# Kernel optimization log

Hardware: AMD Instinct MI355X
Metric: run time of the kernel (lower is better)

Reference implementation:

```python
import jax, jax.numpy as jnp
import numpy as np

# ---- static configuration (matches init_kwargs) ----
D_MODEL = 512
N_HEAD = 16
HEAD_DIM = D_MODEL // N_HEAD
SCALE = HEAD_DIM ** -0.5
SIZE = (64, 64)
WINDOW = (8, 8)
SHIFT = (4, 4)
WS = WINDOW[0] * WINDOW[1]          # tokens per window = 64
NW = (SIZE[0] // WINDOW[0]) * (SIZE[1] // WINDOW[1])  # windows per sample = 64


def _rel_pos_index(window):
    w0, w1 = window
    coords = np.stack(np.meshgrid(np.arange(w0), np.arange(w1), indexing='ij')).reshape(2, -1)
    rel = (coords[:, :, None] - coords[:, None, :]).transpose(1, 2, 0)  # [ws, ws, 2]
    rel[:, :, 0] += w0 - 1
    rel[:, :, 1] += w1 - 1
    rel[:, :, 0] *= 2 * w1 - 1
    return rel.sum(-1)  # [ws, ws] in [0, (2w0-1)(2w1-1))


def _shift_mask(size, window, shift):
    # Swin-style attention mask for shifted windows: 1.0 where tokens belong
    # to different cyclic-shift regions, else 0.0. Shape [nw, ws, ws].
    H, W = size
    w0, w1 = window
    s0, s1 = shift
    img = np.zeros((H, W))
    cnt = 0
    h_slices = (slice(0, -w0), slice(-w0, -s0), slice(-s0, None)) if s0 > 0 else (slice(None),)
    w_slices = (slice(0, -w1), slice(-w1, -s1), slice(-s1, None)) if s1 > 0 else (slice(None),)
    for hs in h_slices:
        for ws_ in w_slices:
            img[hs, ws_] = cnt
            cnt += 1
    win = img.reshape(H // w0, w0, W // w1, w1).transpose(0, 2, 1, 3).reshape(-1, w0 * w1)
    return (win[:, None, :] != win[:, :, None]).astype(np.float32)


REL_IDX = jnp.asarray(_rel_pos_index(WINDOW))              # [ws, ws] int
MASK = jnp.asarray(-100.0 * _shift_mask(SIZE, WINDOW, SHIFT))  # [nw, ws, ws]


def setup_inputs() -> dict:
    key = jax.random.key(0)
    k1, k2, k3, k4 = jax.random.split(key, 4)
    x = jax.random.normal(k1, (8, SIZE[0], SIZE[1], D_MODEL), dtype=jnp.float32)
    qkv_w = jax.random.normal(k2, (3 * D_MODEL, D_MODEL), dtype=jnp.float32) * (D_MODEL ** -0.5)
    qkv_b = jax.random.normal(k3, (3 * D_MODEL,), dtype=jnp.float32) * 0.02
    bias_table = jax.random.normal(k4, ((2 * WINDOW[0] - 1) * (2 * WINDOW[1] - 1), N_HEAD), dtype=jnp.float32) * 0.02
    return {"x": x, "qkv_w": qkv_w, "qkv_b": qkv_b, "bias_table": bias_table}


def reference(x, qkv_w, qkv_b, bias_table):
    n, H, W, c = x.shape
    w0, w1 = WINDOW
    # --- window partition: [n, H, W, c] -> [n*nw, ws, c] ---
    part = x.reshape(n, H // w0, w0, W // w1, w1, c)
    part = part.transpose(0, 1, 3, 2, 4, 5).reshape(n * NW, WS, c)
    # --- qkv projection ---
    qkv = (part @ qkv_w.T + qkv_b).reshape(n * NW, WS, 3, N_HEAD, HEAD_DIM)
    q, k, v = qkv[:, :, 0] * SCALE, qkv[:, :, 1], qkv[:, :, 2]
    # --- scores + relative bias + shift mask + softmax ---
    attn = jnp.einsum('wihd,wjhd->whij', q, k)  # [n*nw, nh, ws, ws]
    bias = bias_table[REL_IDX].transpose(2, 0, 1)  # [nh, ws, ws]
    attn = attn.reshape(n, NW, N_HEAD, WS, WS) + bias[None, None] + MASK[None, :, None]
    attn = jax.nn.softmax(attn, axis=-1).reshape(n * NW, N_HEAD, WS, WS)
    # --- AV + unpartition ---
    out = jnp.einsum('whij,wjhd->wihd', attn, v).reshape(n * NW, WS, c)
    out = out.reshape(n, H // w0, W // w1, w0, w1, c)
    return out.transpose(0, 1, 3, 2, 4, 5).reshape(n, H, W, c)
```

## Files before the change

kernel.cpp:

```cpp
#include <hip/hip_runtime.h>
#include <stdint.h>

typedef unsigned short u16;
typedef __attribute__((ext_vector_type(4))) float floatx4;
typedef __attribute__((ext_vector_type(8))) short bf16x8;

#define MTOK   32768
#define KDIM   512
#define NQKV   1536
#define NWIN   512
#define N_HEAD 16
#define SECSZ  (512 * 16 * 2048)
#define QK_SCALE 0.17677669529663687f

__device__ __forceinline__ u16 f2bf(float f) {
  union { float f; unsigned u; } v; v.f = f;
  unsigned r = v.u + 0x7fffu + ((v.u >> 16) & 1u);
  return (u16)(r >> 16);
}

__device__ __forceinline__ void load_lds16(const void* g, void* l) {
  __builtin_amdgcn_global_load_lds((const __attribute__((address_space(1))) void*)g,
                                   (__attribute__((address_space(3))) void*)l,
                                   16, 0, 0);
}

__global__ __launch_bounds__(256) void convert_xw(const float* __restrict__ x,
                                                  const float* __restrict__ wsrc,
                                                  const float* __restrict__ btab,
                                                  u16* __restrict__ A,
                                                  u16* __restrict__ Wb,
                                                  float* __restrict__ tbl) {
  int b = blockIdx.x;
  if (b < 768) {
    int e = (b * 256 + threadIdx.x) * 4;
    const float4 v = *(const float4*)(wsrc + e);
    ushort4 o;
    o.x = f2bf(v.x); o.y = f2bf(v.y); o.z = f2bf(v.z); o.w = f2bf(v.w);
    *(ushort4*)(Wb + e) = o;
  } else if (b < 17152) {
    int idx = (b - 768) * 256 + threadIdx.x;
    int e = idx * 4;
    int c = e & 511;
    int tg = e >> 9;
    int w = tg >> 6, t = tg & 63;
    int img = w >> 6, wy = (w >> 3) & 7, wx = w & 7;
    int ty = t >> 3, tx = t & 7;
    int y = wy * 8 + ty, xp = wx * 8 + tx;
    const float4 v = *(const float4*)(x + (((img * 64 + y) * 64 + xp) * 512 + c));
    ushort4 o;
    o.x = f2bf(v.x); o.y = f2bf(v.y); o.z = f2bf(v.z); o.w = f2bf(v.w);
    *(ushort4*)(A + e) = o;
  } else {
    int q = b - 17152;
    int cls = q >> 4, hh = q & 15;
    int ey = cls >> 1, ex = cls & 1;
    float* To = tbl + (q << 12);
#pragma unroll
    for (int e = 0; e < 16; ++e) {
      int idx = e * 256 + threadIdx.x;
      int i = idx >> 6, j = idx & 63;
      int ty = i >> 3, tx = i & 7, sy = j >> 3, sx = j & 7;
      int ry = ey ? (ty < 4 ? 1 : 2) : 0;
      int rx = ex ? (tx < 4 ? 1 : 2) : 0;
      int qy = ey ? (sy < 4 ? 1 : 2) : 0;
      int qx = ex ? (sx < 4 ? 1 : 2) : 0;
      float v = btab[((ty - sy + 7) * 15 + (tx - sx + 7)) * 16 + hh];
      if (ry * 3 + rx != qy * 3 + qx) v -= 100.0f;
      To[idx] = v;
    }
  }
}

__global__ __launch_bounds__(256, 4) void gemm_qkv(const u16* __restrict__ A,
                                                   const u16* __restrict__ Wb,
                                                   const float* __restrict__ bias,
                                                   u16* __restrict__ QKV) {
  __shared__ __attribute__((aligned(16))) char smem[18432];
  u16* Ct = (u16*)smem;

  int b = blockIdx.x;
  int xcd = b & 7, slot = b >> 3;
  int mtile = (slot / 12) * 8 + xcd;
  int ntile = slot % 12;

  int tid = threadIdx.x;
  int wv = tid >> 6, lane = tid & 63;
  int il = lane & 15, ch = lane >> 4;
  int wm = (wv & 1) * 64, wn = (wv >> 1) * 64;

  floatx4 acc[4][4];
  floatx4 zacc = {0.f, 0.f, 0.f, 0.f};
#pragma unroll
  for (int m = 0; m < 4; ++m)
#pragma unroll
    for (int n = 0; n < 4; ++n) acc[m][n] = zacc;

  int s8   = (tid & 7) ^ ((tid >> 3) & 7);
  int row0 = ((tid >> 3) << 1) + (s8 >> 2);
  int ch4  = s8 & 3;
  const u16* Abase = A + (mtile * 128 + row0) * KDIM + ch4 * 8;
  const u16* Bbase = Wb + (ntile * 128 + row0) * KDIM + ch4 * 8;
  char* lAb = smem;
  char* lBb = smem + 8192;
  char* lA0 = lAb + wv * 1024;
  char* lA1 = lAb + 4096 + wv * 1024;
  char* lB0 = lBb + wv * 1024;
  char* lB1 = lBb + 4096 + wv * 1024;

  int aslot = ((il & 1) * 4 + ch) ^ ((il >> 1) & 7);
  int fbase = (il >> 1) * 128 + aslot * 16;
  int awoff = (wv & 1) * 4096;
  int bwoff = (wv >> 1) * 4096;

  for (int kb = 0; kb < KDIM; kb += 32) {
    __syncthreads();
    load_lds16(Abase + kb, lA0);
    load_lds16(Abase + kb + 64 * KDIM, lA1);
    load_lds16(Bbase + kb, lB0);
    load_lds16(Bbase + kb + 64 * KDIM, lB1);
    __syncthreads();

    bf16x8 af[4], bfr[4];
#pragma unroll
    for (int mt = 0; mt < 4; ++mt)
      af[mt] = *(const bf16x8*)(lAb + awoff + fbase + mt * 1024);
#pragma unroll
    for (int nt = 0; nt < 4; ++nt)
      bfr[nt] = *(const bf16x8*)(lBb + bwoff + fbase + nt * 1024);
#pragma unroll
    for (int mt = 0; mt < 4; ++mt)
#pragma unroll
      for (int nt = 0; nt < 4; ++nt)
        acc[mt][nt] = __builtin_amdgcn_mfma_f32_16x16x32_bf16(af[mt], bfr[nt], acc[mt][nt], 0, 0, 0);
  }

  __syncthreads();

  int sec = ntile >> 2;
  int h0 = (ntile & 3) * 4;
  int gw0 = mtile * 2;
  u16* dst = QKV + (size_t)sec * SECSZ;
  float sc = (sec == 0) ? QK_SCALE : 1.0f;

  for (int p = 0; p < 2; ++p) {
    if ((wv & 1) == p) {
      if (sec < 2) {
#pragma unroll
        for (int nt = 0; nt < 4; ++nt) {
          float bv = bias[ntile * 128 + wn + nt * 16 + il];
          int cl = wn + nt * 16 + il;
#pragma unroll
          for (int mt = 0; mt < 4; ++mt) {
            int lr = mt * 16 + ch * 4;
#pragma unroll
            for (int r = 0; r < 4; ++r)
              Ct[(lr + r) * 136 + cl] = f2bf((acc[mt][nt][r] + bv) * sc);
          }
        }
      } else {
#pragma unroll
        for (int nt = 0; nt < 4; ++nt) {
          float bv = bias[ntile * 128 + wn + nt * 16 + il];
          int cl = wn + nt * 16 + il;
#pragma unroll
          for (int mt = 0; mt < 4; ++mt) {
            int lr = mt * 16 + ch * 4;
            ushort4 pk;
            pk.x = f2bf(acc[mt][nt][0] + bv);
            pk.y = f2bf(acc[mt][nt][1] + bv);
            pk.z = f2bf(acc[mt][nt][2] + bv);
            pk.w = f2bf(acc[mt][nt][3] + bv);
            *(ushort4*)(Ct + cl * 72 + lr) = pk;
          }
        }
      }
    }
    __syncthreads();

    if (sec < 2) {
      int tl = tid >> 2, dc = tid & 3;
#pragma unroll
      for (int hl = 0; hl < 4; ++hl) {
        uint4 v = *(const uint4*)(smem + tl * 272 + hl * 64 + dc * 16);
        *(uint4*)(dst + ((gw0 + p) * 16 + h0 + hl) * 2048 + tl * 32 + dc * 8) = v;
      }
    } else {
      int c0 = tid >> 3, tq = tid & 7;
#pragma unroll
      for (int hl = 0; hl < 4; ++hl) {
        uint4 v = *(const uint4*)(smem + (hl * 32 + c0) * 144 + tq * 16);
        *(uint4*)(dst + ((gw0 + p) * 16 + h0 + hl) * 2048 + c0 * 64 + tq * 8) = v;
      }
    }
    __syncthreads();
  }
}

__global__ __launch_bounds__(256) void attn(const u16* __restrict__ QKV,
                                            const float* __restrict__ tbl,
                                            float* __restrict__ out) {
  __shared__ __attribute__((aligned(16))) u16 Pl[64 * 88];

  int bid = blockIdx.x;
  int w = bid >> 4, h = bid & 15;
  int tid = threadIdx.x;

  int lane = tid & 63, wv = tid >> 6;
  int il = lane & 15, ch = lane >> 4;
  const u16* Qb = QKV + (w * 16 + h) * 2048;
  const u16* Kb = Qb + SECSZ;
  const u16* Vt = Qb + 2 * (size_t)SECSZ;

  bf16x8 aq = *(const bf16x8*)(Qb + (wv * 16 + il) * 32 + ch * 8);
  floatx4 zacc = {0.f, 0.f, 0.f, 0.f};
  floatx4 s[4];
#pragma unroll
  for (int jt = 0; jt < 4; ++jt) {
    bf16x8 bk = *(const bf16x8*)(Kb + (jt * 16 + il) * 32 + ch * 8);
    s[jt] = __builtin_amdgcn_mfma_f32_16x16x32_bf16(aq, bk, zacc, 0, 0, 0);
  }

  int winidx = w & 63;
  int wy = winidx >> 3, wx = winidx & 7;
  int cls = ((wy == 7) ? 2 : 0) | ((wx == 7) ? 1 : 0);
  const float* T = tbl + (((cls << 4) | h) << 12);

  float val[4][4];
#pragma unroll
  for (int r = 0; r < 4; ++r) {
    int i = wv * 16 + ch * 4 + r;
#pragma unroll
    for (int jt = 0; jt < 4; ++jt)
      val[r][jt] = s[jt][r] + T[i * 64 + jt * 16 + il];
  }

#pragma unroll
  for (int r = 0; r < 4; ++r) {
    float m = fmaxf(fmaxf(val[r][0], val[r][1]), fmaxf(val[r][2], val[r][3]));
    m = fmaxf(m, __shfl_xor(m, 1, 64));
    m = fmaxf(m, __shfl_xor(m, 2, 64));
    m = fmaxf(m, __shfl_xor(m, 4, 64));
    m = fmaxf(m, __shfl_xor(m, 8, 64));
    float sum = 0.f;
#pragma unroll
    for (int jt = 0; jt < 4; ++jt) { val[r][jt] = __expf(val[r][jt] - m); sum += val[r][jt]; }
    sum += __shfl_xor(sum, 1, 64);
    sum += __shfl_xor(sum, 2, 64);
    sum += __shfl_xor(sum, 4, 64);
    sum += __shfl_xor(sum, 8, 64);
    float inv = 1.0f / sum;
    int i = wv * 16 + ch * 4 + r;
#pragma unroll
    for (int jt = 0; jt < 4; ++jt)
      Pl[i * 88 + jt * 16 + il] = f2bf(val[r][jt] * inv);
  }

  __syncthreads();

  floatx4 o0 = zacc, o1 = zacc;
#pragma unroll
  for (int kk = 0; kk < 2; ++kk) {
    bf16x8 ap  = *(const bf16x8*)((const u16*)Pl + (wv * 16 + il) * 88 + kk * 32 + ch * 8);
    bf16x8 bv0 = *(const bf16x8*)(Vt + il * 64 + kk * 32 + ch * 8);
    bf16x8 bv1 = *(const bf16x8*)(Vt + (16 + il) * 64 + kk * 32 + ch * 8);
    o0 = __builtin_amdgcn_mfma_f32_16x16x32_bf16(ap, bv0, o0, 0, 0, 0);
    o1 = __builtin_amdgcn_mfma_f32_16x16x32_bf16(ap, bv1, o1, 0, 0, 0);
  }

  int img = w >> 6;
#pragma unroll
  for (int r = 0; r < 4; ++r) {
    int i = wv * 16 + ch * 4 + r;
    int ty = i >> 3, tx = i & 7;
    int y = wy * 8 + ty, xp = wx * 8 + tx;
    float* op = out + ((img * 64 + y) * 64 + xp) * 512 + h * 32;
    op[il] = o0[r];
    op[16 + il] = o1[r];
  }
}

extern "C" void kernel_launch(void* const* d_in, const int* in_sizes, int n_in,
                              void* d_out, int out_size, void* d_ws, size_t ws_size,
                              hipStream_t stream) {
  const float* x      = (const float*)d_in[0];
  const float* qkv_w  = (const float*)d_in[1];
  const float* qkv_b  = (const float*)d_in[2];
  const float* btab   = (const float*)d_in[3];
  float* out = (float*)d_out;

  char* ws = (char*)d_ws;
  u16* A    = (u16*)ws;
  u16* Wb   = (u16*)(ws + (size_t)MTOK * KDIM * 2);
  u16* QKV  = (u16*)(ws + (size_t)MTOK * KDIM * 2 + (size_t)NQKV * KDIM * 2);
  float* tbl = (float*)(ws + (size_t)MTOK * KDIM * 2 + (size_t)NQKV * KDIM * 2
                           + 3 * (size_t)SECSZ * 2);

  convert_xw<<<dim3(17216), dim3(256), 0, stream>>>(x, qkv_w, btab, A, Wb, tbl);
  gemm_qkv<<<dim3(3072), dim3(256), 0, stream>>>(A, Wb, qkv_b, QKV);
  attn<<<dim3(NWIN * N_HEAD), dim3(256), 0, stream>>>(QKV, tbl, out);
}
```

Measured before the change: 226.9 us.

## Fuse x window-partition and bf16 conversion into QKV GEMM A-tile load

Removes the separate pass that gathered x into windowed order and converted it to bf16. The GEMM now reads fp32 x directly with the window-partition indexing, converts to bf16 in registers and writes the A tile to LDS with an XOR swizzle. B still uses async global-to-LDS loads. This avoids writing and re-reading a 32 MB bf16 staging buffer, at the cost of reading fp32 x once per N-tile (12 times), doing synchronous register loads, and converting inside the GEMM main loop.

```diff
diff --git a/kernel.cpp b/kernel.cpp
--- a/kernel.cpp
+++ b/kernel.cpp
@@ -25,12 +25,10 @@
                                    16, 0, 0);
 }
 
-__global__ __launch_bounds__(256) void convert_xw(const float* __restrict__ x,
-                                                  const float* __restrict__ wsrc,
-                                                  const float* __restrict__ btab,
-                                                  u16* __restrict__ A,
-                                                  u16* __restrict__ Wb,
-                                                  float* __restrict__ tbl) {
+__global__ __launch_bounds__(256) void convert_w_tbl(const float* __restrict__ wsrc,
+                                                     const float* __restrict__ btab,
+                                                     u16* __restrict__ Wb,
+                                                     float* __restrict__ tbl) {
   int b = blockIdx.x;
   if (b < 768) {
     int e = (b * 256 + threadIdx.x) * 4;
@@ -38,21 +36,8 @@
     ushort4 o;
     o.x = f2bf(v.x); o.y = f2bf(v.y); o.z = f2bf(v.z); o.w = f2bf(v.w);
     *(ushort4*)(Wb + e) = o;
-  } else if (b < 17152) {
-    int idx = (b - 768) * 256 + threadIdx.x;
-    int e = idx * 4;
-    int c = e & 511;
-    int tg = e >> 9;
-    int w = tg >> 6, t = tg & 63;
-    int img = w >> 6, wy = (w >> 3) & 7, wx = w & 7;
-    int ty = t >> 3, tx = t & 7;
-    int y = wy * 8 + ty, xp = wx * 8 + tx;
-    const float4 v = *(const float4*)(x + (((img * 64 + y) * 64 + xp) * 512 + c));
-    ushort4 o;
-    o.x = f2bf(v.x); o.y = f2bf(v.y); o.z = f2bf(v.z); o.w = f2bf(v.w);
-    *(ushort4*)(A + e) = o;
   } else {
-    int q = b - 17152;
+    int q = b - 768;
     int cls = q >> 4, hh = q & 15;
     int ey = cls >> 1, ex = cls & 1;
     float* To = tbl + (q << 12);
@@ -72,7 +57,7 @@
   }
 }
 
-__global__ __launch_bounds__(256, 4) void gemm_qkv(const u16* __restrict__ A,
+__global__ __launch_bounds__(256, 4) void gemm_qkv(const float* __restrict__ x,
                                                    const u16* __restrict__ Wb,
                                                    const float* __restrict__ bias,
                                                    u16* __restrict__ QKV) {
@@ -96,38 +81,52 @@
 #pragma unroll
     for (int n = 0; n < 4; ++n) acc[m][n] = zacc;
 
-  int s8   = (tid & 7) ^ ((tid >> 3) & 7);
-  int row0 = ((tid >> 3) << 1) + (s8 >> 2);
-  int ch4  = s8 & 3;
-  const u16* Abase = A + (mtile * 128 + row0) * KDIM + ch4 * 8;
+  int row0 = tid >> 2;
+  int ch4 = (tid & 3) ^ (row0 & 3);
+  int T0 = mtile * 128 + row0;
+  int T1 = T0 + 64;
+  int w0 = T0 >> 6, t0 = T0 & 63;
+  int w1 = T1 >> 6, t1 = T1 & 63;
+  const float* px0 = x + ((((w0 >> 6) * 64 + ((w0 >> 3) & 7) * 8 + (t0 >> 3)) * 64
+                           + (w0 & 7) * 8 + (t0 & 7)) * 512 + ch4 * 8);
+  const float* px1 = x + ((((w1 >> 6) * 64 + ((w1 >> 3) & 7) * 8 + (t1 >> 3)) * 64
+                           + (w1 & 7) * 8 + (t1 & 7)) * 512 + ch4 * 8);
+
   const u16* Bbase = Wb + (ntile * 128 + row0) * KDIM + ch4 * 8;
-  char* lAb = smem;
   char* lBb = smem + 8192;
-  char* lA0 = lAb + wv * 1024;
-  char* lA1 = lAb + 4096 + wv * 1024;
   char* lB0 = lBb + wv * 1024;
   char* lB1 = lBb + 4096 + wv * 1024;
-
-  int aslot = ((il & 1) * 4 + ch) ^ ((il >> 1) & 7);
-  int fbase = (il >> 1) * 128 + aslot * 16;
-  int awoff = (wv & 1) * 4096;
-  int bwoff = (wv >> 1) * 4096;
-
+  char* lAb = smem;
+
+  int sw = il & 3;
   for (int kb = 0; kb < KDIM; kb += 32) {
     __syncthreads();
-    load_lds16(Abase + kb, lA0);
-    load_lds16(Abase + kb + 64 * KDIM, lA1);
     load_lds16(Bbase + kb, lB0);
     load_lds16(Bbase + kb + 64 * KDIM, lB1);
+    float4 a00 = *(const float4*)(px0 + kb);
+    float4 a01 = *(const float4*)(px0 + kb + 4);
+    float4 a10 = *(const float4*)(px1 + kb);
+    float4 a11 = *(const float4*)(px1 + kb + 4);
+    bf16x8 p0, p1;
+    p0[0] = (short)f2bf(a00.x); p0[1] = (short)f2bf(a00.y);
+    p0[2] = (short)f2bf(a00.z); p0[3] = (short)f2bf(a00.w);
+    p0[4] = (short)f2bf(a01.x); p0[5] = (short)f2bf(a01.y);
+    p0[6] = (short)f2bf(a01.z); p0[7] = (short)f2bf(a01.w);
+    p1[0] = (short)f2bf(a10.x); p1[1] = (short)f2bf(a10.y);
+    p1[2] = (short)f2bf(a10.z); p1[3] = (short)f2bf(a10.w);
+    p1[4] = (short)f2bf(a11.x); p1[5] = (short)f2bf(a11.y);
+    p1[6] = (short)f2bf(a11.z); p1[7] = (short)f2bf(a11.w);
+    *(bf16x8*)(lAb + tid * 16) = p0;
+    *(bf16x8*)(lAb + 4096 + tid * 16) = p1;
     __syncthreads();
 
     bf16x8 af[4], bfr[4];
 #pragma unroll
     for (int mt = 0; mt < 4; ++mt)
-      af[mt] = *(const bf16x8*)(lAb + awoff + fbase + mt * 1024);
+      af[mt] = *(const bf16x8*)(lAb + (wm + mt * 16 + il) * 64 + (ch ^ sw) * 16);
 #pragma unroll
     for (int nt = 0; nt < 4; ++nt)
-      bfr[nt] = *(const bf16x8*)(lBb + bwoff + fbase + nt * 1024);
+      bfr[nt] = *(const bf16x8*)(lBb + (wn + nt * 16 + il) * 64 + (ch ^ sw) * 16);
 #pragma unroll
     for (int mt = 0; mt < 4; ++mt)
 #pragma unroll
@@ -290,13 +289,11 @@
   float* out = (float*)d_out;
 
   char* ws = (char*)d_ws;
-  u16* A    = (u16*)ws;
-  u16* Wb   = (u16*)(ws + (size_t)MTOK * KDIM * 2);
-  u16* QKV  = (u16*)(ws + (size_t)MTOK * KDIM * 2 + (size_t)NQKV * KDIM * 2);
-  float* tbl = (float*)(ws + (size_t)MTOK * KDIM * 2 + (size_t)NQKV * KDIM * 2
-                           + 3 * (size_t)SECSZ * 2);
-
-  convert_xw<<<dim3(17216), dim3(256), 0, stream>>>(x, qkv_w, btab, A, Wb, tbl);
-  gemm_qkv<<<dim3(3072), dim3(256), 0, stream>>>(A, Wb, qkv_b, QKV);
+  u16* Wb    = (u16*)ws;
+  u16* QKV   = (u16*)(ws + (size_t)NQKV * KDIM * 2);
+  float* tbl = (float*)(ws + (size_t)NQKV * KDIM * 2 + 3 * (size_t)SECSZ * 2);
+
+  convert_w_tbl<<<dim3(832), dim3(256), 0, stream>>>(qkv_w, btab, Wb, tbl);
+  gemm_qkv<<<dim3(3072), dim3(256), 0, stream>>>(x, Wb, qkv_b, QKV);
   attn<<<dim3(NWIN * N_HEAD), dim3(256), 0, stream>>>(QKV, tbl, out);
 }
```

After: 234.8 us. 1.03x slower.

## Process all heads per window in one attention block and simplify GEMM LDS swizzle

Applied to the files above, without the earlier changes.

The attention kernel now launches one block per window, with each wave looping over four heads and using a private LDS slice for probabilities, so the block-level barrier is gone and launch count drops. The QKV GEMM switches to a simpler row-major LDS layout with a 4-chunk XOR swizzle for the fragment reads. The aim is to cut per-block overhead and address arithmetic. In exchange, attention parallelism falls to 512 blocks with serialized per-wave work, which may reduce latency hiding, and the new swizzle may alter bank-conflict behaviour.

```diff
diff --git a/kernel.cpp b/kernel.cpp
--- a/kernel.cpp
+++ b/kernel.cpp
@@ -96,9 +96,8 @@
 #pragma unroll
     for (int n = 0; n < 4; ++n) acc[m][n] = zacc;
 
-  int s8   = (tid & 7) ^ ((tid >> 3) & 7);
-  int row0 = ((tid >> 3) << 1) + (s8 >> 2);
-  int ch4  = s8 & 3;
+  int row0 = tid >> 2;
+  int ch4 = (tid & 3) ^ (row0 & 3);
   const u16* Abase = A + (mtile * 128 + row0) * KDIM + ch4 * 8;
   const u16* Bbase = Wb + (ntile * 128 + row0) * KDIM + ch4 * 8;
   char* lAb = smem;
@@ -108,11 +107,7 @@
   char* lB0 = lBb + wv * 1024;
   char* lB1 = lBb + 4096 + wv * 1024;
 
-  int aslot = ((il & 1) * 4 + ch) ^ ((il >> 1) & 7);
-  int fbase = (il >> 1) * 128 + aslot * 16;
-  int awoff = (wv & 1) * 4096;
-  int bwoff = (wv >> 1) * 4096;
-
+  int sw = il & 3;
   for (int kb = 0; kb < KDIM; kb += 32) {
     __syncthreads();
     load_lds16(Abase + kb, lA0);
@@ -124,10 +119,10 @@
     bf16x8 af[4], bfr[4];
 #pragma unroll
     for (int mt = 0; mt < 4; ++mt)
-      af[mt] = *(const bf16x8*)(lAb + awoff + fbase + mt * 1024);
+      af[mt] = *(const bf16x8*)(lAb + (wm + mt * 16 + il) * 64 + (ch ^ sw) * 16);
 #pragma unroll
     for (int nt = 0; nt < 4; ++nt)
-      bfr[nt] = *(const bf16x8*)(lBb + bwoff + fbase + nt * 1024);
+      bfr[nt] = *(const bf16x8*)(lBb + (wn + nt * 16 + il) * 64 + (ch ^ sw) * 16);
 #pragma unroll
     for (int mt = 0; mt < 4; ++mt)
 #pragma unroll
@@ -200,83 +195,95 @@
 __global__ __launch_bounds__(256) void attn(const u16* __restrict__ QKV,
                                             const float* __restrict__ tbl,
                                             float* __restrict__ out) {
-  __shared__ __attribute__((aligned(16))) u16 Pl[64 * 88];
-
-  int bid = blockIdx.x;
-  int w = bid >> 4, h = bid & 15;
+  __shared__ __attribute__((aligned(16))) u16 Pl[4 * 64 * 88];
+
+  int w = blockIdx.x;
   int tid = threadIdx.x;
-
   int lane = tid & 63, wv = tid >> 6;
   int il = lane & 15, ch = lane >> 4;
-  const u16* Qb = QKV + (w * 16 + h) * 2048;
-  const u16* Kb = Qb + SECSZ;
-  const u16* Vt = Qb + 2 * (size_t)SECSZ;
-
-  bf16x8 aq = *(const bf16x8*)(Qb + (wv * 16 + il) * 32 + ch * 8);
-  floatx4 zacc = {0.f, 0.f, 0.f, 0.f};
-  floatx4 s[4];
-#pragma unroll
-  for (int jt = 0; jt < 4; ++jt) {
-    bf16x8 bk = *(const bf16x8*)(Kb + (jt * 16 + il) * 32 + ch * 8);
-    s[jt] = __builtin_amdgcn_mfma_f32_16x16x32_bf16(aq, bk, zacc, 0, 0, 0);
-  }
 
   int winidx = w & 63;
   int wy = winidx >> 3, wx = winidx & 7;
   int cls = ((wy == 7) ? 2 : 0) | ((wx == 7) ? 1 : 0);
-  const float* T = tbl + (((cls << 4) | h) << 12);
-
-  float val[4][4];
-#pragma unroll
-  for (int r = 0; r < 4; ++r) {
-    int i = wv * 16 + ch * 4 + r;
-#pragma unroll
-    for (int jt = 0; jt < 4; ++jt)
-      val[r][jt] = s[jt][r] + T[i * 64 + jt * 16 + il];
-  }
-
-#pragma unroll
-  for (int r = 0; r < 4; ++r) {
-    float m = fmaxf(fmaxf(val[r][0], val[r][1]), fmaxf(val[r][2], val[r][3]));
-    m = fmaxf(m, __shfl_xor(m, 1, 64));
-    m = fmaxf(m, __shfl_xor(m, 2, 64));
-    m = fmaxf(m, __shfl_xor(m, 4, 64));
-    m = fmaxf(m, __shfl_xor(m, 8, 64));
-    float sum = 0.f;
-#pragma unroll
-    for (int jt = 0; jt < 4; ++jt) { val[r][jt] = __expf(val[r][jt] - m); sum += val[r][jt]; }
-    sum += __shfl_xor(sum, 1, 64);
-    sum += __shfl_xor(sum, 2, 64);
-    sum += __shfl_xor(sum, 4, 64);
-    sum += __shfl_xor(sum, 8, 64);
-    float inv = 1.0f / sum;
-    int i = wv * 16 + ch * 4 + r;
-#pragma unroll
-    for (int jt = 0; jt < 4; ++jt)
-      Pl[i * 88 + jt * 16 + il] = f2bf(val[r][jt] * inv);
-  }
-
-  __syncthreads();
-
-  floatx4 o0 = zacc, o1 = zacc;
-#pragma unroll
-  for (int kk = 0; kk < 2; ++kk) {
-    bf16x8 ap  = *(const bf16x8*)((const u16*)Pl + (wv * 16 + il) * 88 + kk * 32 + ch * 8);
-    bf16x8 bv0 = *(const bf16x8*)(Vt + il * 64 + kk * 32 + ch * 8);
-    bf16x8 bv1 = *(const bf16x8*)(Vt + (16 + il) * 64 + kk * 32 + ch * 8);
-    o0 = __builtin_amdgcn_mfma_f32_16x16x32_bf16(ap, bv0, o0, 0, 0, 0);
-    o1 = __builtin_amdgcn_mfma_f32_16x16x32_bf16(ap, bv1, o1, 0, 0, 0);
-  }
-
   int img = w >> 6;
-#pragma unroll
-  for (int r = 0; r < 4; ++r) {
-    int i = wv * 16 + ch * 4 + r;
-    int ty = i >> 3, tx = i & 7;
-    int y = wy * 8 + ty, xp = wx * 8 + tx;
-    float* op = out + ((img * 64 + y) * 64 + xp) * 512 + h * 32;
-    op[il] = o0[r];
-    op[16 + il] = o1[r];
+
+  u16* Pw = Pl + wv * (64 * 88);
+  floatx4 zacc = {0.f, 0.f, 0.f, 0.f};
+
+  for (int q = 0; q < 4; ++q) {
+    int h = wv * 4 + q;
+    const u16* Qb = QKV + (w * 16 + h) * 2048;
+    const u16* Kb = Qb + SECSZ;
+    const u16* Vt = Qb + 2 * (size_t)SECSZ;
+    const float* T = tbl + (((cls << 4) | h) << 12);
+
+    bf16x8 aq[4], bk[4], bv[2][2];
+#pragma unroll
+    for (int i = 0; i < 4; ++i) {
+      aq[i] = *(const bf16x8*)(Qb + (i * 16 + il) * 32 + ch * 8);
+      bk[i] = *(const bf16x8*)(Kb + (i * 16 + il) * 32 + ch * 8);
+    }
+#pragma unroll
+    for (int kk = 0; kk < 2; ++kk) {
+      bv[kk][0] = *(const bf16x8*)(Vt + il * 64 + kk * 32 + ch * 8);
+      bv[kk][1] = *(const bf16x8*)(Vt + (16 + il) * 64 + kk * 32 + ch * 8);
+    }
+
+    floatx4 s[4][4];
+#pragma unroll
+    for (int i = 0; i < 4; ++i)
+#pragma unroll
+      for (int j = 0; j < 4; ++j)
+        s[i][j] = __builtin_amdgcn_mfma_f32_16x16x32_bf16(aq[i], bk[j], zacc, 0, 0, 0);
+
+#pragma unroll
+    for (int i = 0; i < 4; ++i) {
+#pragma unroll
+      for (int r = 0; r < 4; ++r) {
+        int row = i * 16 + ch * 4 + r;
+        float v0 = s[i][0][r] + T[row * 64 + il];
+        float v1 = s[i][1][r] + T[row * 64 + 16 + il];
+        float v2 = s[i][2][r] + T[row * 64 + 32 + il];
+        float v3 = s[i][3][r] + T[row * 64 + 48 + il];
+        float m = fmaxf(fmaxf(v0, v1), fmaxf(v2, v3));
+        m = fmaxf(m, __shfl_xor(m, 1, 64));
+        m = fmaxf(m, __shfl_xor(m, 2, 64));
+        m = fmaxf(m, __shfl_xor(m, 4, 64));
+        m = fmaxf(m, __shfl_xor(m, 8, 64));
+        v0 = __expf(v0 - m); v1 = __expf(v1 - m);
+        v2 = __expf(v2 - m); v3 = __expf(v3 - m);
+        float sum = v0 + v1 + v2 + v3;
+        sum += __shfl_xor(sum, 1, 64);
+        sum += __shfl_xor(sum, 2, 64);
+        sum += __shfl_xor(sum, 4, 64);
+        sum += __shfl_xor(sum, 8, 64);
+        float inv = 1.0f / sum;
+        Pw[row * 88 + il]      = f2bf(v0 * inv);
+        Pw[row * 88 + 16 + il] = f2bf(v1 * inv);
+        Pw[row * 88 + 32 + il] = f2bf(v2 * inv);
+        Pw[row * 88 + 48 + il] = f2bf(v3 * inv);
+      }
+    }
+
+#pragma unroll
+    for (int i = 0; i < 4; ++i) {
+      floatx4 o0 = zacc, o1 = zacc;
+#pragma unroll
+      for (int kk = 0; kk < 2; ++kk) {
+        bf16x8 ap = *(const bf16x8*)(Pw + (i * 16 + il) * 88 + kk * 32 + ch * 8);
+        o0 = __builtin_amdgcn_mfma_f32_16x16x32_bf16(ap, bv[kk][0], o0, 0, 0, 0);
+        o1 = __builtin_amdgcn_mfma_f32_16x16x32_bf16(ap, bv[kk][1], o1, 0, 0, 0);
+      }
+#pragma unroll
+      for (int r = 0; r < 4; ++r) {
+        int t = i * 16 + ch * 4 + r;
+        int ty = t >> 3, tx = t & 7;
+        int y = wy * 8 + ty, xp = wx * 8 + tx;
+        float* op = out + ((img * 64 + y) * 64 + xp) * 512 + h * 32;
+        op[il] = o0[r];
+        op[16 + il] = o1[r];
+      }
+    }
   }
 }
 
@@ -298,5 +305,5 @@
 
   convert_xw<<<dim3(17216), dim3(256), 0, stream>>>(x, qkv_w, btab, A, Wb, tbl);
   gemm_qkv<<<dim3(3072), dim3(256), 0, stream>>>(A, Wb, qkv_b, QKV);
-  attn<<<dim3(NWIN * N_HEAD), dim3(256), 0, stream>>>(QKV, tbl, out);
-}
+  attn<<<dim3(NWIN), dim3(256), 0, stream>>>(QKV, tbl, out);
+}
```

New measurement: 249.0 us. +9.8%, slower.

## Simplify GEMM LDS swizzle, split QKV GEMM launches, prefetch V in attention

Applied to the files above, without the earlier changes.

The QKV GEMM's LDS staging moves to a simpler row-major layout with a 4-way XOR swizzle on 16-byte chunks. This replaces the earlier paired-row swizzle and is meant to cut LDS bank conflicts and address arithmetic. The GEMM is also split into four launches of 768 blocks, each covering a quarter of the M tiles through a new mbase argument, which adds launch overhead. In the attention kernel, the V fragments are loaded from global memory before the softmax so their latency overlaps it. The block-wide __syncthreads before the P·V step becomes a wave-local lgkmcnt wait, which is valid because each wave reads back only the P rows it wrote.

```diff
diff --git a/kernel.cpp b/kernel.cpp
--- a/kernel.cpp
+++ b/kernel.cpp
@@ -75,13 +75,14 @@
 __global__ __launch_bounds__(256, 4) void gemm_qkv(const u16* __restrict__ A,
                                                    const u16* __restrict__ Wb,
                                                    const float* __restrict__ bias,
-                                                   u16* __restrict__ QKV) {
+                                                   u16* __restrict__ QKV,
+                                                   int mbase) {
   __shared__ __attribute__((aligned(16))) char smem[18432];
   u16* Ct = (u16*)smem;
 
   int b = blockIdx.x;
   int xcd = b & 7, slot = b >> 3;
-  int mtile = (slot / 12) * 8 + xcd;
+  int mtile = mbase + (slot / 12) * 8 + xcd;
   int ntile = slot % 12;
 
   int tid = threadIdx.x;
@@ -96,9 +97,8 @@
 #pragma unroll
     for (int n = 0; n < 4; ++n) acc[m][n] = zacc;
 
-  int s8   = (tid & 7) ^ ((tid >> 3) & 7);
-  int row0 = ((tid >> 3) << 1) + (s8 >> 2);
-  int ch4  = s8 & 3;
+  int row0 = tid >> 2;
+  int ch4 = (tid & 3) ^ (row0 & 3);
   const u16* Abase = A + (mtile * 128 + row0) * KDIM + ch4 * 8;
   const u16* Bbase = Wb + (ntile * 128 + row0) * KDIM + ch4 * 8;
   char* lAb = smem;
@@ -108,11 +108,7 @@
   char* lB0 = lBb + wv * 1024;
   char* lB1 = lBb + 4096 + wv * 1024;
 
-  int aslot = ((il & 1) * 4 + ch) ^ ((il >> 1) & 7);
-  int fbase = (il >> 1) * 128 + aslot * 16;
-  int awoff = (wv & 1) * 4096;
-  int bwoff = (wv >> 1) * 4096;
-
+  int sw = il & 3;
   for (int kb = 0; kb < KDIM; kb += 32) {
     __syncthreads();
     load_lds16(Abase + kb, lA0);
@@ -124,10 +120,10 @@
     bf16x8 af[4], bfr[4];
 #pragma unroll
     for (int mt = 0; mt < 4; ++mt)
-      af[mt] = *(const bf16x8*)(lAb + awoff + fbase + mt * 1024);
+      af[mt] = *(const bf16x8*)(lAb + (wm + mt * 16 + il) * 64 + (ch ^ sw) * 16);
 #pragma unroll
     for (int nt = 0; nt < 4; ++nt)
-      bfr[nt] = *(const bf16x8*)(lBb + bwoff + fbase + nt * 1024);
+      bfr[nt] = *(const bf16x8*)(lBb + (wn + nt * 16 + il) * 64 + (ch ^ sw) * 16);
 #pragma unroll
     for (int mt = 0; mt < 4; ++mt)
 #pragma unroll
@@ -221,6 +217,13 @@
     s[jt] = __builtin_amdgcn_mfma_f32_16x16x32_bf16(aq, bk, zacc, 0, 0, 0);
   }
 
+  bf16x8 bv0[2], bv1[2];
+#pragma unroll
+  for (int kk = 0; kk < 2; ++kk) {
+    bv0[kk] = *(const bf16x8*)(Vt + il * 64 + kk * 32 + ch * 8);
+    bv1[kk] = *(const bf16x8*)(Vt + (16 + il) * 64 + kk * 32 + ch * 8);
+  }
+
   int winidx = w & 63;
   int wy = winidx >> 3, wx = winidx & 7;
   int cls = ((wy == 7) ? 2 : 0) | ((wx == 7) ? 1 : 0);
@@ -256,16 +259,15 @@
       Pl[i * 88 + jt * 16 + il] = f2bf(val[r][jt] * inv);
   }
 
-  __syncthreads();
+  asm volatile("s_waitcnt lgkmcnt(0)" ::: "memory");
+  __builtin_amdgcn_sched_barrier(0);
 
   floatx4 o0 = zacc, o1 = zacc;
 #pragma unroll
   for (int kk = 0; kk < 2; ++kk) {
-    bf16x8 ap  = *(const bf16x8*)((const u16*)Pl + (wv * 16 + il) * 88 + kk * 32 + ch * 8);
-    bf16x8 bv0 = *(const bf16x8*)(Vt + il * 64 + kk * 32 + ch * 8);
-    bf16x8 bv1 = *(const bf16x8*)(Vt + (16 + il) * 64 + kk * 32 + ch * 8);
-    o0 = __builtin_amdgcn_mfma_f32_16x16x32_bf16(ap, bv0, o0, 0, 0, 0);
-    o1 = __builtin_amdgcn_mfma_f32_16x16x32_bf16(ap, bv1, o1, 0, 0, 0);
+    bf16x8 ap = *(const bf16x8*)((const u16*)Pl + (wv * 16 + il) * 88 + kk * 32 + ch * 8);
+    o0 = __builtin_amdgcn_mfma_f32_16x16x32_bf16(ap, bv0[kk], o0, 0, 0, 0);
+    o1 = __builtin_amdgcn_mfma_f32_16x16x32_bf16(ap, bv1[kk], o1, 0, 0, 0);
   }
 
   int img = w >> 6;
@@ -297,6 +299,9 @@
                            + 3 * (size_t)SECSZ * 2);
 
   convert_xw<<<dim3(17216), dim3(256), 0, stream>>>(x, qkv_w, btab, A, Wb, tbl);
-  gemm_qkv<<<dim3(3072), dim3(256), 0, stream>>>(A, Wb, qkv_b, QKV);
+  gemm_qkv<<<dim3(768), dim3(256), 0, stream>>>(A, Wb, qkv_b, QKV, 0);
+  gemm_qkv<<<dim3(768), dim3(256), 0, stream>>>(A, Wb, qkv_b, QKV, 64);
+  gemm_qkv<<<dim3(768), dim3(256), 0, stream>>>(A, Wb, qkv_b, QKV, 128);
+  gemm_qkv<<<dim3(768), dim3(256), 0, stream>>>(A, Wb, qkv_b, QKV, 192);
   attn<<<dim3(NWIN * N_HEAD), dim3(256), 0, stream>>>(QKV, tbl, out);
 }
```

Result: slower. 238.6 us (+5.1%).
